# Kernel tuning notes

Hardware: AMD Instinct MI355X
Metric: run time of the kernel (lower is better)

Reference implementation:

```python
import jax, jax.numpy as jnp
import numpy as np

N_NODES = 50000
N_EDGES = 800000
HIDDEN = 64
NUM_FEATURES = 1
OUT_DIM = 2


def setup_inputs() -> dict:
    key = jax.random.key(0)
    k = jax.random.split(key, 6)
    x = jax.random.normal(k[0], (N_NODES, NUM_FEATURES), dtype=jnp.float32)
    edge_index = jax.random.randint(k[1], (2, N_EDGES), 0, N_NODES, dtype=jnp.int32)
    # GCNConv params (PyG default: glorot weight, zero bias; random here for testing)
    W1 = jax.random.normal(k[2], (NUM_FEATURES, HIDDEN), dtype=jnp.float32) * 0.5
    b1 = jax.random.normal(k[3], (HIDDEN,), dtype=jnp.float32) * 0.1
    W2 = jax.random.normal(k[4], (HIDDEN, OUT_DIM), dtype=jnp.float32) * 0.1
    b2 = jax.random.normal(k[5], (OUT_DIM,), dtype=jnp.float32) * 0.1
    return {"x": x, "edge_index": edge_index, "W1": W1, "b1": b1, "W2": W2, "b2": b2}


def _gcn_norm(edge_index, num_nodes):
    # PyG gcn_norm with add_self_loops=True, symmetric normalization
    row, col = edge_index[0], edge_index[1]
    loop = jnp.arange(num_nodes, dtype=row.dtype)
    row = jnp.concatenate([row, loop])
    col = jnp.concatenate([col, loop])
    ew = jnp.ones(row.shape[0], dtype=jnp.float32)
    deg = jax.ops.segment_sum(ew, col, num_segments=num_nodes)  # in-degree incl. self-loop
    dinv = jnp.where(deg > 0, jax.lax.rsqrt(deg), 0.0)
    norm = dinv[row] * dinv[col]  # [E+N]
    return row, col, norm


def _gcn_conv(x, row, col, norm, W, b, num_nodes):
    h = x @ W                                  # [N, out] transform first (out <= in here is fine)
    msg = h[row] * norm[:, None]               # gather + scale, [E+N, out]
    out = jax.ops.segment_sum(msg, col, num_segments=num_nodes)  # scatter-add at targets
    return out + b


def reference(x, edge_index, W1, b1, W2, b2):
    row, col, norm = _gcn_norm(edge_index, N_NODES)
    h = _gcn_conv(x, row, col, norm, W1, b1, N_NODES)
    h = jax.nn.relu(h)
    out = _gcn_conv(h, row, col, norm, W2, b2, N_NODES)
    return out
```

## Files before the change

kernel.cpp:

```cpp
#include <hip/hip_runtime.h>
#include <math.h>

#define N_NODES 50000
#define N_EDGES 800000
#define HIDDEN  64
#define MAXDEG  64


__global__ void k_build(const int* __restrict__ row, const int* __restrict__ col,
                        int* __restrict__ cnt, unsigned short* __restrict__ ell) {
    int e = blockIdx.x * blockDim.x + threadIdx.x;
    if (e < N_EDGES) {
        int c = col[e];
        int rk = atomicAdd(&cnt[c], 1);
        if (rk < MAXDEG) ell[rk * N_NODES + c] = (unsigned short)row[e];
    }
}

__global__ void k_dinvg(const int* __restrict__ cnt, const float* __restrict__ x,
                        float* __restrict__ dinv, float* __restrict__ g) {
    int i = blockIdx.x * blockDim.x + threadIdx.x;
    if (i < N_NODES) {
        float di = rsqrtf((float)(cnt[i] + 1));
        dinv[i] = di;
        g[i] = di * x[i];
    }
}

__global__ void k_layer1(const unsigned short* __restrict__ ell,
                         const int* __restrict__ cnt, const float* __restrict__ g,
                         const float* __restrict__ dinv,
                         const float* __restrict__ W1, const float* __restrict__ b1,
                         const float* __restrict__ W2, float2* __restrict__ z) {
    int n = blockIdx.x * blockDim.x + threadIdx.x;
    if (n >= N_NODES) return;
    int d = cnt[n]; if (d > MAXDEG) d = MAXDEG;
    float acc = 0.0f;
    int j = 0;
    for (; j + 2 <= d; j += 2) {
        int r0 = ell[j * N_NODES + n];
        int r1 = ell[(j + 1) * N_NODES + n];
        acc += g[r0] + g[r1];
    }
    if (j < d) acc += g[ell[j * N_NODES + n]];
    float di = dinv[n];
    float sv = di * (acc + g[n]);
    float y0 = 0.0f, y1 = 0.0f;
#pragma unroll
    for (int k = 0; k < HIDDEN; ++k) {
        float h = fmaxf(sv * W1[k] + b1[k], 0.0f);
        y0 += h * W2[2 * k];
        y1 += h * W2[2 * k + 1];
    }
    z[n] = make_float2(di * y0, di * y1);
}

__global__ void k_layer2(const unsigned short* __restrict__ ell,
                         const int* __restrict__ cnt, const float2* __restrict__ z,
                         const float* __restrict__ dinv, const float* __restrict__ b2,
                         float* __restrict__ out) {
    int n = blockIdx.x * blockDim.x + threadIdx.x;
    if (n >= N_NODES) return;
    int d = cnt[n]; if (d > MAXDEG) d = MAXDEG;
    float T0 = 0.0f, T1 = 0.0f;
    int j = 0;
    for (; j + 2 <= d; j += 2) {
        int r0 = ell[j * N_NODES + n];
        int r1 = ell[(j + 1) * N_NODES + n];
        float2 v0 = z[r0], v1 = z[r1];
        T0 += v0.x + v1.x;
        T1 += v0.y + v1.y;
    }
    if (j < d) {
        float2 v = z[ell[j * N_NODES + n]];
        T0 += v.x; T1 += v.y;
    }
    float di = dinv[n];
    float2 zn = z[n];
    out[2 * n]     = di * (T0 + zn.x) + b2[0];
    out[2 * n + 1] = di * (T1 + zn.y) + b2[1];
}


extern "C" void kernel_launch(void* const* d_in, const int* in_sizes, int n_in,
                              void* d_out, int out_size, void* d_ws, size_t ws_size,
                              hipStream_t stream) {
    const float* x  = (const float*)d_in[0];
    const int*   ei = (const int*)d_in[1];
    const float* W1 = (const float*)d_in[2];
    const float* b1 = (const float*)d_in[3];
    const float* W2 = (const float*)d_in[4];
    const float* b2 = (const float*)d_in[5];
    float* out = (float*)d_out;

    const int* row = ei;
    const int* col = ei + N_EDGES;

    int*    ws   = (int*)d_ws;
    int*    cnt  = ws;
    float*  dinv = (float*)(ws + 1 * N_NODES);
    float*  g    = (float*)(ws + 2 * N_NODES);
    float2* z    = (float2*)(ws + 3 * N_NODES);
    unsigned short* ell = (unsigned short*)(ws + 5 * N_NODES);

    const int BE = 256, BN = 128;
    const int gE = (N_EDGES + BE - 1) / BE;
    const int gN = (N_NODES + BN - 1) / BN;

    hipMemsetAsync(cnt, 0, N_NODES * sizeof(int), stream);
    k_build<<<gE, BE, 0, stream>>>(row, col, cnt, ell);
    k_dinvg<<<gN, BN, 0, stream>>>(cnt, x, dinv, g);
    k_layer1<<<gN, BN, 0, stream>>>(ell, cnt, g, dinv, W1, b1, W2, z);
    k_layer2<<<gN, BN, 0, stream>>>(ell, cnt, z, dinv, b2, out);
}
```

Baseline: 127.8 us.

## Replace ELL build with chunked sliced LDS-atomic aggregation and partial-sum reduction

```diff
diff --git a/kernel.cpp b/kernel.cpp
--- a/kernel.cpp
+++ b/kernel.cpp
@@ -1,14 +1,146 @@
 #include <hip/hip_runtime.h>
 #include <math.h>
 
-#define N_NODES 50000
-#define N_EDGES 800000
-#define HIDDEN  64
-#define MAXDEG  64
-
-
-__global__ void k_build(const int* __restrict__ row, const int* __restrict__ col,
-                        int* __restrict__ cnt, unsigned short* __restrict__ ell) {
+#define N_NODES  50000
+#define N_EDGES  800000
+#define HIDDEN   64
+#define C_CHUNKS 32
+#define S_SLICES 32
+#define CHUNK    (N_EDGES / C_CHUNKS)
+#define CHUNK4   (CHUNK / 4)
+#define SLICE    ((N_NODES + S_SLICES - 1) / S_SLICES)
+
+
+__global__ __launch_bounds__(256)
+void k_hist(const int* __restrict__ col, int* __restrict__ part_cnt) {
+    const int c  = blockIdx.x % C_CHUNKS;
+    const int s  = blockIdx.x / C_CHUNKS;
+    const int lo = s * SLICE;
+    const int len = min(SLICE, N_NODES - lo);
+    __shared__ int h[SLICE];
+    for (int i = threadIdx.x; i < len; i += 256) h[i] = 0;
+    __syncthreads();
+    const int4* col4 = (const int4*)(col + c * CHUNK);
+    for (int i = threadIdx.x; i < CHUNK4; i += 256) {
+        int4 v = col4[i];
+        unsigned a = (unsigned)(v.x - lo); if (a < (unsigned)len) atomicAdd(&h[a], 1);
+        unsigned b = (unsigned)(v.y - lo); if (b < (unsigned)len) atomicAdd(&h[b], 1);
+        unsigned d = (unsigned)(v.z - lo); if (d < (unsigned)len) atomicAdd(&h[d], 1);
+        unsigned e = (unsigned)(v.w - lo); if (e < (unsigned)len) atomicAdd(&h[e], 1);
+    }
+    __syncthreads();
+    int* dst = part_cnt + c * N_NODES + lo;
+    for (int i = threadIdx.x; i < len; i += 256) dst[i] = h[i];
+}
+
+__global__ void k_dinvg(const int* __restrict__ part_cnt, const float* __restrict__ x,
+                        float* __restrict__ dinv, float* __restrict__ g) {
+    int n = blockIdx.x * blockDim.x + threadIdx.x;
+    if (n >= N_NODES) return;
+    int deg = 0;
+#pragma unroll
+    for (int c = 0; c < C_CHUNKS; ++c) deg += part_cnt[c * N_NODES + n];
+    float di = rsqrtf((float)(deg + 1));
+    dinv[n] = di;
+    g[n] = di * x[n];
+}
+
+__global__ __launch_bounds__(256)
+void k_agg1(const int* __restrict__ row, const int* __restrict__ col,
+            const float* __restrict__ g, float* __restrict__ part_t) {
+    const int c  = blockIdx.x % C_CHUNKS;
+    const int s  = blockIdx.x / C_CHUNKS;
+    const int lo = s * SLICE;
+    const int len = min(SLICE, N_NODES - lo);
+    __shared__ float acc[SLICE];
+    for (int i = threadIdx.x; i < len; i += 256) acc[i] = 0.0f;
+    __syncthreads();
+    const int4* col4 = (const int4*)(col + c * CHUNK);
+    const int4* row4 = (const int4*)(row + c * CHUNK);
+    for (int i = threadIdx.x; i < CHUNK4; i += 256) {
+        int4 cv = col4[i];
+        int4 rv = row4[i];
+        unsigned a = (unsigned)(cv.x - lo); if (a < (unsigned)len) atomicAdd(&acc[a], g[rv.x]);
+        unsigned b = (unsigned)(cv.y - lo); if (b < (unsigned)len) atomicAdd(&acc[b], g[rv.y]);
+        unsigned d = (unsigned)(cv.z - lo); if (d < (unsigned)len) atomicAdd(&acc[d], g[rv.z]);
+        unsigned e = (unsigned)(cv.w - lo); if (e < (unsigned)len) atomicAdd(&acc[e], g[rv.w]);
+    }
+    __syncthreads();
+    float* dst = part_t + c * N_NODES + lo;
+    for (int i = threadIdx.x; i < len; i += 256) dst[i] = acc[i];
+}
+
+__global__ void k_mlp(const float* __restrict__ part_t, const float* __restrict__ g,
+                      const float* __restrict__ dinv,
+                      const float* __restrict__ W1, const float* __restrict__ b1,
+                      const float* __restrict__ W2, float2* __restrict__ z) {
+    int n = blockIdx.x * blockDim.x + threadIdx.x;
+    if (n >= N_NODES) return;
+    float t = 0.0f;
+#pragma unroll
+    for (int c = 0; c < C_CHUNKS; ++c) t += part_t[c * N_NODES + n];
+    float di = dinv[n];
+    float sv = di * (t + g[n]);
+    float y0 = 0.0f, y1 = 0.0f;
+#pragma unroll
+    for (int k = 0; k < HIDDEN; ++k) {
+        float h = fmaxf(sv * W1[k] + b1[k], 0.0f);
+        y0 += h * W2[2 * k];
+        y1 += h * W2[2 * k + 1];
+    }
+    z[n] = make_float2(di * y0, di * y1);
+}
+
+__global__ __launch_bounds__(256)
+void k_agg2(const int* __restrict__ row, const int* __restrict__ col,
+            const float2* __restrict__ z, float2* __restrict__ part_z) {
+    const int c  = blockIdx.x % C_CHUNKS;
+    const int s  = blockIdx.x / C_CHUNKS;
+    const int lo = s * SLICE;
+    const int len = min(SLICE, N_NODES - lo);
+    __shared__ float accx[SLICE];
+    __shared__ float accy[SLICE];
+    for (int i = threadIdx.x; i < len; i += 256) { accx[i] = 0.0f; accy[i] = 0.0f; }
+    __syncthreads();
+    const int4* col4 = (const int4*)(col + c * CHUNK);
+    const int4* row4 = (const int4*)(row + c * CHUNK);
+    for (int i = threadIdx.x; i < CHUNK4; i += 256) {
+        int4 cv = col4[i];
+        int4 rv = row4[i];
+        unsigned a = (unsigned)(cv.x - lo);
+        if (a < (unsigned)len) { float2 v = z[rv.x]; atomicAdd(&accx[a], v.x); atomicAdd(&accy[a], v.y); }
+        unsigned b = (unsigned)(cv.y - lo);
+        if (b < (unsigned)len) { float2 v = z[rv.y]; atomicAdd(&accx[b], v.x); atomicAdd(&accy[b], v.y); }
+        unsigned d = (unsigned)(cv.z - lo);
+        if (d < (unsigned)len) { float2 v = z[rv.z]; atomicAdd(&accx[d], v.x); atomicAdd(&accy[d], v.y); }
+        unsigned e = (unsigned)(cv.w - lo);
+        if (e < (unsigned)len) { float2 v = z[rv.w]; atomicAdd(&accx[e], v.x); atomicAdd(&accy[e], v.y); }
+    }
+    __syncthreads();
+    float2* dst = part_z + c * N_NODES + lo;
+    for (int i = threadIdx.x; i < len; i += 256) dst[i] = make_float2(accx[i], accy[i]);
+}
+
+__global__ void k_final(const float2* __restrict__ part_z, const float2* __restrict__ z,
+                        const float* __restrict__ dinv, const float* __restrict__ b2,
+                        float2* __restrict__ out) {
+    int n = blockIdx.x * blockDim.x + threadIdx.x;
+    if (n >= N_NODES) return;
+    float T0 = 0.0f, T1 = 0.0f;
+#pragma unroll
+    for (int c = 0; c < C_CHUNKS; ++c) {
+        float2 v = part_z[c * N_NODES + n];
+        T0 += v.x; T1 += v.y;
+    }
+    float di = dinv[n];
+    float2 zn = z[n];
+    out[n] = make_float2(di * (T0 + zn.x) + b2[0], di * (T1 + zn.y) + b2[1]);
+}
+
+
+#define MAXDEG 64
+__global__ void fb_build(const int* __restrict__ row, const int* __restrict__ col,
+                         int* __restrict__ cnt, unsigned short* __restrict__ ell) {
     int e = blockIdx.x * blockDim.x + threadIdx.x;
     if (e < N_EDGES) {
         int c = col[e];
@@ -16,9 +148,8 @@
         if (rk < MAXDEG) ell[rk * N_NODES + c] = (unsigned short)row[e];
     }
 }
-
-__global__ void k_dinvg(const int* __restrict__ cnt, const float* __restrict__ x,
-                        float* __restrict__ dinv, float* __restrict__ g) {
+__global__ void fb_dinvg(const int* __restrict__ cnt, const float* __restrict__ x,
+                         float* __restrict__ dinv, float* __restrict__ g) {
     int i = blockIdx.x * blockDim.x + threadIdx.x;
     if (i < N_NODES) {
         float di = rsqrtf((float)(cnt[i] + 1));
@@ -26,23 +157,15 @@
         g[i] = di * x[i];
     }
 }
-
-__global__ void k_layer1(const unsigned short* __restrict__ ell,
-                         const int* __restrict__ cnt, const float* __restrict__ g,
-                         const float* __restrict__ dinv,
-                         const float* __restrict__ W1, const float* __restrict__ b1,
-                         const float* __restrict__ W2, float2* __restrict__ z) {
+__global__ void fb_layer1(const unsigned short* __restrict__ ell, const int* __restrict__ cnt,
+                          const float* __restrict__ g, const float* __restrict__ dinv,
+                          const float* __restrict__ W1, const float* __restrict__ b1,
+                          const float* __restrict__ W2, float2* __restrict__ z) {
     int n = blockIdx.x * blockDim.x + threadIdx.x;
     if (n >= N_NODES) return;
     int d = cnt[n]; if (d > MAXDEG) d = MAXDEG;
     float acc = 0.0f;
-    int j = 0;
-    for (; j + 2 <= d; j += 2) {
-        int r0 = ell[j * N_NODES + n];
-        int r1 = ell[(j + 1) * N_NODES + n];
-        acc += g[r0] + g[r1];
-    }
-    if (j < d) acc += g[ell[j * N_NODES + n]];
+    for (int j = 0; j < d; ++j) acc += g[ell[j * N_NODES + n]];
     float di = dinv[n];
     float sv = di * (acc + g[n]);
     float y0 = 0.0f, y1 = 0.0f;
@@ -54,24 +177,14 @@
     }
     z[n] = make_float2(di * y0, di * y1);
 }
-
-__global__ void k_layer2(const unsigned short* __restrict__ ell,
-                         const int* __restrict__ cnt, const float2* __restrict__ z,
-                         const float* __restrict__ dinv, const float* __restrict__ b2,
-                         float* __restrict__ out) {
+__global__ void fb_layer2(const unsigned short* __restrict__ ell, const int* __restrict__ cnt,
+                          const float2* __restrict__ z, const float* __restrict__ dinv,
+                          const float* __restrict__ b2, float* __restrict__ out) {
     int n = blockIdx.x * blockDim.x + threadIdx.x;
     if (n >= N_NODES) return;
     int d = cnt[n]; if (d > MAXDEG) d = MAXDEG;
     float T0 = 0.0f, T1 = 0.0f;
-    int j = 0;
-    for (; j + 2 <= d; j += 2) {
-        int r0 = ell[j * N_NODES + n];
-        int r1 = ell[(j + 1) * N_NODES + n];
-        float2 v0 = z[r0], v1 = z[r1];
-        T0 += v0.x + v1.x;
-        T1 += v0.y + v1.y;
-    }
-    if (j < d) {
+    for (int j = 0; j < d; ++j) {
         float2 v = z[ell[j * N_NODES + n]];
         T0 += v.x; T1 += v.y;
     }
@@ -91,25 +204,43 @@
     const float* b1 = (const float*)d_in[3];
     const float* W2 = (const float*)d_in[4];
     const float* b2 = (const float*)d_in[5];
-    float* out = (float*)d_out;
 
     const int* row = ei;
     const int* col = ei + N_EDGES;
 
-    int*    ws   = (int*)d_ws;
-    int*    cnt  = ws;
-    float*  dinv = (float*)(ws + 1 * N_NODES);
-    float*  g    = (float*)(ws + 2 * N_NODES);
-    float2* z    = (float2*)(ws + 3 * N_NODES);
-    unsigned short* ell = (unsigned short*)(ws + 5 * N_NODES);
-
-    const int BE = 256, BN = 128;
-    const int gE = (N_EDGES + BE - 1) / BE;
-    const int gN = (N_NODES + BN - 1) / BN;
-
-    hipMemsetAsync(cnt, 0, N_NODES * sizeof(int), stream);
-    k_build<<<gE, BE, 0, stream>>>(row, col, cnt, ell);
-    k_dinvg<<<gN, BN, 0, stream>>>(cnt, x, dinv, g);
-    k_layer1<<<gN, BN, 0, stream>>>(ell, cnt, g, dinv, W1, b1, W2, z);
-    k_layer2<<<gN, BN, 0, stream>>>(ell, cnt, z, dinv, b2, out);
-}
+    const size_t need = (size_t)(4 * N_NODES + 4 * C_CHUNKS * N_NODES) * 4;
+
+    if (ws_size >= need) {
+        char* p = (char*)d_ws;
+        float*  dinv     = (float*)p;                 p += N_NODES * 4;
+        float*  g        = (float*)p;                 p += N_NODES * 4;
+        float2* z        = (float2*)p;                p += N_NODES * 8;
+        int*    part_cnt = (int*)p;                   p += (size_t)C_CHUNKS * N_NODES * 4;
+        float*  part_t   = (float*)p;                 p += (size_t)C_CHUNKS * N_NODES * 4;
+        float2* part_z   = (float2*)p;
+
+        const int gS = C_CHUNKS * S_SLICES;
+        const int gN = (N_NODES + 255) / 256;
+
+        k_hist <<<gS, 256, 0, stream>>>(col, part_cnt);
+        k_dinvg<<<gN, 256, 0, stream>>>(part_cnt, x, dinv, g);
+        k_agg1 <<<gS, 256, 0, stream>>>(row, col, g, part_t);
+        k_mlp  <<<gN, 256, 0, stream>>>(part_t, g, dinv, W1, b1, W2, z);
+        k_agg2 <<<gS, 256, 0, stream>>>(row, col, z, part_z);
+        k_final<<<gN, 256, 0, stream>>>(part_z, z, dinv, b2, (float2*)d_out);
+    } else {
+        int*    ws   = (int*)d_ws;
+        int*    cnt  = ws;
+        float*  dinv = (float*)(ws + 1 * N_NODES);
+        float*  g    = (float*)(ws + 2 * N_NODES);
+        float2* z    = (float2*)(ws + 3 * N_NODES);
+        unsigned short* ell = (unsigned short*)(ws + 5 * N_NODES);
+        const int gE = (N_EDGES + 255) / 256;
+        const int gN = (N_NODES + 127) / 128;
+        hipMemsetAsync(cnt, 0, N_NODES * sizeof(int), stream);
+        fb_build <<<gE, 256, 0, stream>>>(row, col, cnt, ell);
+        fb_dinvg <<<gN, 128, 0, stream>>>(cnt, x, dinv, g);
+        fb_layer1<<<gN, 128, 0, stream>>>(ell, cnt, g, dinv, W1, b1, W2, z);
+        fb_layer2<<<gN, 128, 0, stream>>>(ell, cnt, z, dinv, b2, (float*)d_out);
+    }
+}
```

Result: slower. 141.6 us (+10.8%).

## Replace ELL build with bucketed edge partitioning and LDS atomic aggregation

Applied to the files above, without the earlier changes.

```diff
diff --git a/kernel.cpp b/kernel.cpp
--- a/kernel.cpp
+++ b/kernel.cpp
@@ -4,47 +4,136 @@
 #define N_NODES 50000
 #define N_EDGES 800000
 #define HIDDEN  64
-#define MAXDEG  64
-
-
-__global__ void k_build(const int* __restrict__ row, const int* __restrict__ col,
-                        int* __restrict__ cnt, unsigned short* __restrict__ ell) {
-    int e = blockIdx.x * blockDim.x + threadIdx.x;
-    if (e < N_EDGES) {
-        int c = col[e];
-        int rk = atomicAdd(&cnt[c], 1);
-        if (rk < MAXDEG) ell[rk * N_NODES + c] = (unsigned short)row[e];
-    }
-}
-
-__global__ void k_dinvg(const int* __restrict__ cnt, const float* __restrict__ x,
-                        float* __restrict__ dinv, float* __restrict__ g) {
-    int i = blockIdx.x * blockDim.x + threadIdx.x;
-    if (i < N_NODES) {
-        float di = rsqrtf((float)(cnt[i] + 1));
-        dinv[i] = di;
-        g[i] = di * x[i];
-    }
-}
-
-__global__ void k_layer1(const unsigned short* __restrict__ ell,
-                         const int* __restrict__ cnt, const float* __restrict__ g,
-                         const float* __restrict__ dinv,
-                         const float* __restrict__ W1, const float* __restrict__ b1,
-                         const float* __restrict__ W2, float2* __restrict__ z) {
-    int n = blockIdx.x * blockDim.x + threadIdx.x;
+#define NBUCK   32
+#define SLICE   1568
+#define BCAP    26500
+#define NBB     64
+#define EPB     (N_EDGES / NBB)
+#define TILE    2048
+#define NSUB    8
+#define NGROUP  (N_NODES / 4)
+
+
+__global__ __launch_bounds__(256)
+void k_bucket(const int* __restrict__ row, const int* __restrict__ col,
+              unsigned* __restrict__ tails, unsigned* __restrict__ histPart,
+              unsigned* __restrict__ bks) {
+    __shared__ unsigned hist[NGROUP];
+    __shared__ unsigned stage[TILE];
+    __shared__ unsigned char sbuck[TILE];
+    __shared__ unsigned cntb[NBUCK], baseb[NBUCK], cnt2[NBUCK], gpos[NBUCK];
+    const int t  = threadIdx.x;
+    const int e0 = blockIdx.x * EPB;
+
+    for (int i = t; i < NGROUP; i += 256) hist[i] = 0u;
+
+    for (int tile = 0; tile < EPB; tile += TILE) {
+        const int cnt = min(TILE, EPB - tile);
+        if (t < NBUCK) { cntb[t] = 0u; cnt2[t] = 0u; }
+        __syncthreads();
+
+        int myc[8], myr[8], mb[8];
+#pragma unroll
+        for (int k = 0; k < 8; ++k) {
+            int ii = k * 256 + t;
+            mb[k] = -1;
+            if (ii < cnt) {
+                int c = col[e0 + tile + ii];
+                int r = row[e0 + tile + ii];
+                myc[k] = c; myr[k] = r;
+                int b = c / SLICE;
+                mb[k] = b;
+                atomicAdd(&cntb[b], 1u);
+                atomicAdd(&hist[c >> 2], 1u << ((c & 3) * 8));
+            }
+        }
+        __syncthreads();
+        if (t == 0) {
+            unsigned acc = 0;
+            for (int b = 0; b < NBUCK; ++b) { baseb[b] = acc; acc += cntb[b]; }
+        }
+        __syncthreads();
+#pragma unroll
+        for (int k = 0; k < 8; ++k) {
+            if (mb[k] >= 0) {
+                unsigned off = atomicAdd(&cnt2[mb[k]], 1u);
+                unsigned pos = baseb[mb[k]] + off;
+                stage[pos] = ((unsigned)(myc[k] % SLICE) << 16) | (unsigned)myr[k];
+                sbuck[pos] = (unsigned char)mb[k];
+            }
+        }
+        __syncthreads();
+        if (t < NBUCK) gpos[t] = atomicAdd(&tails[t], cntb[t]);
+        __syncthreads();
+        for (int i = t; i < cnt; i += 256) {
+            int b = sbuck[i];
+            unsigned dst = gpos[b] + ((unsigned)i - baseb[b]);
+            if (dst < BCAP) bks[(size_t)b * BCAP + dst] = stage[i];
+        }
+        __syncthreads();
+    }
+    unsigned* hp = histPart + (size_t)blockIdx.x * NGROUP;
+    for (int i = t; i < NGROUP; i += 256) hp[i] = hist[i];
+}
+
+__global__ __launch_bounds__(256)
+void k_g(const unsigned* __restrict__ histPart, const float* __restrict__ x,
+         float* __restrict__ dinv, float* __restrict__ g) {
+    int i = blockIdx.x * 256 + threadIdx.x;
+    if (i >= NGROUP) return;
+    unsigned sum = 0;
+    for (int b0 = 0; b0 < NBB; b0 += 8) {
+        unsigned v[8];
+#pragma unroll
+        for (int k = 0; k < 8; ++k) v[k] = histPart[(size_t)(b0 + k) * NGROUP + i];
+#pragma unroll
+        for (int k = 0; k < 8; ++k) sum += v[k];
+    }
+    int n0 = i * 4;
+#pragma unroll
+    for (int b = 0; b < 4; ++b) {
+        int deg = (int)((sum >> (8 * b)) & 255u);
+        float di = rsqrtf((float)(deg + 1));
+        dinv[n0 + b] = di;
+        g[n0 + b] = di * x[n0 + b];
+    }
+}
+
+__global__ __launch_bounds__(256)
+void k_agg1(const unsigned* __restrict__ bks, const unsigned* __restrict__ tails,
+            const float* __restrict__ g, float* __restrict__ part1) {
+    __shared__ float acc[SLICE];
+    const int b = blockIdx.x >> 3;
+    const int s = blockIdx.x & (NSUB - 1);
+    for (int i = threadIdx.x; i < SLICE; i += 256) acc[i] = 0.0f;
+    __syncthreads();
+    unsigned tail = min(tails[b], (unsigned)BCAP);
+    unsigned chunk = (tail + NSUB - 1) / NSUB;
+    unsigned lo = s * chunk, hi = min(lo + chunk, tail);
+    const unsigned* bk = bks + (size_t)b * BCAP;
+    for (unsigned i = lo + threadIdx.x; i < hi; i += 256) {
+        unsigned v = bk[i];
+        atomicAdd(&acc[v >> 16], g[v & 0xFFFFu]);
+    }
+    __syncthreads();
+    float* dst = part1 + ((size_t)b * NSUB + s) * SLICE;
+    for (int i = threadIdx.x; i < SLICE; i += 256) dst[i] = acc[i];
+}
+
+__global__ __launch_bounds__(256)
+void k_mlp(const float* __restrict__ part1, const float* __restrict__ g,
+           const float* __restrict__ dinv,
+           const float* __restrict__ W1, const float* __restrict__ b1,
+           const float* __restrict__ W2, float2* __restrict__ z) {
+    int n = blockIdx.x * 256 + threadIdx.x;
     if (n >= N_NODES) return;
-    int d = cnt[n]; if (d > MAXDEG) d = MAXDEG;
-    float acc = 0.0f;
-    int j = 0;
-    for (; j + 2 <= d; j += 2) {
-        int r0 = ell[j * N_NODES + n];
-        int r1 = ell[(j + 1) * N_NODES + n];
-        acc += g[r0] + g[r1];
-    }
-    if (j < d) acc += g[ell[j * N_NODES + n]];
+    int b = n / SLICE, cl = n % SLICE;
+    const float* p = part1 + (size_t)b * NSUB * SLICE + cl;
+    float t = 0.0f;
+#pragma unroll
+    for (int s = 0; s < NSUB; ++s) t += p[(size_t)s * SLICE];
     float di = dinv[n];
-    float sv = di * (acc + g[n]);
+    float sv = di * (t + g[n]);
     float y0 = 0.0f, y1 = 0.0f;
 #pragma unroll
     for (int k = 0; k < HIDDEN; ++k) {
@@ -55,30 +144,44 @@
     z[n] = make_float2(di * y0, di * y1);
 }
 
-__global__ void k_layer2(const unsigned short* __restrict__ ell,
-                         const int* __restrict__ cnt, const float2* __restrict__ z,
-                         const float* __restrict__ dinv, const float* __restrict__ b2,
-                         float* __restrict__ out) {
-    int n = blockIdx.x * blockDim.x + threadIdx.x;
+__global__ __launch_bounds__(256)
+void k_agg2(const unsigned* __restrict__ bks, const unsigned* __restrict__ tails,
+            const float2* __restrict__ z, float2* __restrict__ part2) {
+    __shared__ float accx[SLICE];
+    __shared__ float accy[SLICE];
+    const int b = blockIdx.x >> 3;
+    const int s = blockIdx.x & (NSUB - 1);
+    for (int i = threadIdx.x; i < SLICE; i += 256) { accx[i] = 0.0f; accy[i] = 0.0f; }
+    __syncthreads();
+    unsigned tail = min(tails[b], (unsigned)BCAP);
+    unsigned chunk = (tail + NSUB - 1) / NSUB;
+    unsigned lo = s * chunk, hi = min(lo + chunk, tail);
+    const unsigned* bk = bks + (size_t)b * BCAP;
+    for (unsigned i = lo + threadIdx.x; i < hi; i += 256) {
+        unsigned v = bk[i];
+        float2 zz = z[v & 0xFFFFu];
+        atomicAdd(&accx[v >> 16], zz.x);
+        atomicAdd(&accy[v >> 16], zz.y);
+    }
+    __syncthreads();
+    float2* dst = part2 + ((size_t)b * NSUB + s) * SLICE;
+    for (int i = threadIdx.x; i < SLICE; i += 256) dst[i] = make_float2(accx[i], accy[i]);
+}
+
+__global__ __launch_bounds__(256)
+void k_final(const float2* __restrict__ part2, const float2* __restrict__ z,
+             const float* __restrict__ dinv, const float* __restrict__ b2,
+             float2* __restrict__ out) {
+    int n = blockIdx.x * 256 + threadIdx.x;
     if (n >= N_NODES) return;
-    int d = cnt[n]; if (d > MAXDEG) d = MAXDEG;
-    float T0 = 0.0f, T1 = 0.0f;
-    int j = 0;
-    for (; j + 2 <= d; j += 2) {
-        int r0 = ell[j * N_NODES + n];
-        int r1 = ell[(j + 1) * N_NODES + n];
-        float2 v0 = z[r0], v1 = z[r1];
-        T0 += v0.x + v1.x;
-        T1 += v0.y + v1.y;
-    }
-    if (j < d) {
-        float2 v = z[ell[j * N_NODES + n]];
-        T0 += v.x; T1 += v.y;
-    }
+    int b = n / SLICE, cl = n % SLICE;
+    const float2* p = part2 + (size_t)b * NSUB * SLICE + cl;
+    float Tx = 0.0f, Ty = 0.0f;
+#pragma unroll
+    for (int s = 0; s < NSUB; ++s) { float2 v = p[(size_t)s * SLICE]; Tx += v.x; Ty += v.y; }
     float di = dinv[n];
     float2 zn = z[n];
-    out[2 * n]     = di * (T0 + zn.x) + b2[0];
-    out[2 * n + 1] = di * (T1 + zn.y) + b2[1];
+    out[n] = make_float2(di * (Tx + zn.x) + b2[0], di * (Ty + zn.y) + b2[1]);
 }
 
 
@@ -91,25 +194,29 @@
     const float* b1 = (const float*)d_in[3];
     const float* W2 = (const float*)d_in[4];
     const float* b2 = (const float*)d_in[5];
-    float* out = (float*)d_out;
 
     const int* row = ei;
     const int* col = ei + N_EDGES;
 
-    int*    ws   = (int*)d_ws;
-    int*    cnt  = ws;
-    float*  dinv = (float*)(ws + 1 * N_NODES);
-    float*  g    = (float*)(ws + 2 * N_NODES);
-    float2* z    = (float2*)(ws + 3 * N_NODES);
-    unsigned short* ell = (unsigned short*)(ws + 5 * N_NODES);
-
-    const int BE = 256, BN = 128;
-    const int gE = (N_EDGES + BE - 1) / BE;
-    const int gN = (N_NODES + BN - 1) / BN;
-
-    hipMemsetAsync(cnt, 0, N_NODES * sizeof(int), stream);
-    k_build<<<gE, BE, 0, stream>>>(row, col, cnt, ell);
-    k_dinvg<<<gN, BN, 0, stream>>>(cnt, x, dinv, g);
-    k_layer1<<<gN, BN, 0, stream>>>(ell, cnt, g, dinv, W1, b1, W2, z);
-    k_layer2<<<gN, BN, 0, stream>>>(ell, cnt, z, dinv, b2, out);
-}
+    char* p = (char*)d_ws;
+    unsigned* tails    = (unsigned*)p;                     p += 64 * 4;
+    unsigned* histPart = (unsigned*)p;                     p += (size_t)NBB * NGROUP * 4;
+    unsigned* bks      = (unsigned*)p;                     p += (size_t)NBUCK * BCAP * 4;
+    float*    part1    = (float*)p;                        p += (size_t)NBUCK * NSUB * SLICE * 4;
+    float2*   part2    = (float2*)p;                       p += (size_t)NBUCK * NSUB * SLICE * 8;
+    float*    dinv     = (float*)p;                        p += N_NODES * 4;
+    float*    g        = (float*)p;                        p += N_NODES * 4;
+    float2*   z        = (float2*)p;
+
+    const int gG = (NGROUP + 255) / 256;
+    const int gN = (N_NODES + 255) / 256;
+    const int gA = NBUCK * NSUB;
+
+    hipMemsetAsync(tails, 0, 64 * sizeof(unsigned), stream);
+    k_bucket<<<NBB, 256, 0, stream>>>(row, col, tails, histPart, bks);
+    k_g     <<<gG,  256, 0, stream>>>(histPart, x, dinv, g);
+    k_agg1  <<<gA,  256, 0, stream>>>(bks, tails, g, part1);
+    k_mlp   <<<gN,  256, 0, stream>>>(part1, g, dinv, W1, b1, W2, z);
+    k_agg2  <<<gA,  256, 0, stream>>>(bks, tails, z, part2);
+    k_final <<<gN,  256, 0, stream>>>(part2, z, dinv, b2, (float2*)d_out);
+}
```

Result: slower. 133.3 us (+4.3%).
